# Optimization experiments

Measured on AMD Instinct MI355X. Metric: run time of the kernel, lower is better.

## Reference

```python
import jax, jax.numpy as jnp
import numpy as np

B, C, H, W = 16, 256, 64, 64
NH = 4                      # num_heads
HD = C // NH                # head_dim = 64
G = 32                      # GroupNorm groups
EPS = 1e-5


def setup_inputs() -> dict:
    key = jax.random.key(0)
    ks = jax.random.split(key, 7)
    x = jax.random.normal(ks[0], (B, C, H, W), dtype=jnp.float32)
    gn_w = jnp.ones((C,), dtype=jnp.float32)
    gn_b = jnp.zeros((C,), dtype=jnp.float32)
    qkv_w = jax.random.normal(ks[1], (3 * C, C), dtype=jnp.float32) * 0.02
    qkv_b = jnp.zeros((3 * C,), dtype=jnp.float32)
    out_w = jax.random.normal(ks[2], (C, C), dtype=jnp.float32) * 0.02
    out_b = jnp.zeros((C,), dtype=jnp.float32)
    return {"x": x, "gn_w": gn_w, "gn_b": gn_b, "qkv_w": qkv_w,
            "qkv_b": qkv_b, "out_w": out_w, "out_b": out_b}


def _group_norm(x, w, b):
    # x: (B, C, H, W); normalize over each of G groups of channels (+ spatial)
    Bx, Cx, Hx, Wx = x.shape
    xr = x.reshape(Bx, G, -1)
    mean = xr.mean(axis=-1, keepdims=True)
    var = xr.var(axis=-1, keepdims=True)
    h = ((xr - mean) * jax.lax.rsqrt(var + EPS)).reshape(Bx, Cx, Hx, Wx)
    return h * w[None, :, None, None] + b[None, :, None, None]


def reference(x, gn_w, gn_b, qkv_w, qkv_b, out_w, out_b):
    Bx, Cx, Hx, Wx = x.shape
    N = Hx * Wx
    h = _group_norm(x, gn_w, gn_b)
    # 1x1 conv == channel matmul
    qkv = jnp.einsum('oc,bchw->bohw', qkv_w, h) + qkv_b[None, :, None, None]
    q, k, v = jnp.split(qkv, 3, axis=1)
    # b (h d) y x -> b h d n
    q = q.reshape(Bx, NH, HD, N)
    k = k.reshape(Bx, NH, HD, N)
    v = v.reshape(Bx, NH, HD, N)
    q = jax.nn.softmax(q, axis=-1)   # over spatial positions n
    k = jax.nn.softmax(k, axis=-2)   # over head_dim d
    # context = k @ v^T : (b,h,d,d)
    context = jnp.einsum('bhdn,bhen->bhde', k, v)
    # out = context^T @ q : (b,h,d,n)
    out = jnp.einsum('bhde,bhdn->bhen', context, q)
    out = out.reshape(Bx, Cx, Hx, Wx)
    out = jnp.einsum('oc,bchw->bohw', out_w, out) + out_b[None, :, None, None]
    return x + out
```

## Files before the change

### kernel.cpp

```cpp
#include <hip/hip_runtime.h>


typedef __bf16 bf16x8 __attribute__((ext_vector_type(8)));
typedef __bf16 bf16x4 __attribute__((ext_vector_type(4)));
typedef __bf16 bf16x2 __attribute__((ext_vector_type(2)));
typedef float  f32x4  __attribute__((ext_vector_type(4)));

__device__ __forceinline__ float wave_red_sum(float v) {
#pragma unroll
    for (int off = 32; off > 0; off >>= 1) v += __shfl_xor(v, off, 64);
    return v;
}
__device__ __forceinline__ float wave_red_max(float v) {
#pragma unroll
    for (int off = 32; off > 0; off >>= 1) v = fmaxf(v, __shfl_xor(v, off, 64));
    return v;
}

__global__ __launch_bounds__(256)
void gn_stats_kernel(const float* __restrict__ x, const float* __restrict__ gw,
                     const float* __restrict__ gb, const float* __restrict__ qw,
                     float2* __restrict__ scsh, __bf16* __restrict__ wb)
{
    const int blk = blockIdx.x;
    const int b = blk >> 5, g = blk & 31;
    const int tid = threadIdx.x;
    const int lane = tid & 63, wid = tid >> 6;
    const size_t xbase = ((size_t)(b * 256 + g * 8)) * 4096;

    {
        const int ci = (blk * 256 + tid) * 2;
        if (ci < 196608) {
            const float2 f = *(const float2*)(qw + ci);
            bf16x2 t; t[0] = (__bf16)f.x; t[1] = (__bf16)f.y;
            *(bf16x2*)(wb + ci) = t;
        }
    }

    float s1 = 0.f, s2 = 0.f;
#pragma unroll
    for (int it = 0; it < 32; it++) {
        const int idx = (it * 256 + tid) * 4;
        const float4 v4 = *(const float4*)(x + xbase + idx);
        s1 += v4.x + v4.y + v4.z + v4.w;
        s2 += v4.x * v4.x + v4.y * v4.y + v4.z * v4.z + v4.w * v4.w;
    }
    __shared__ float red[8];
    float s1w = wave_red_sum(s1);
    float s2w = wave_red_sum(s2);
    if (lane == 0) { red[wid] = s1w; red[4 + wid] = s2w; }
    __syncthreads();
    const float mean = (red[0] + red[1] + red[2] + red[3]) * (1.0f / 32768.0f);
    const float ms   = (red[4] + red[5] + red[6] + red[7]) * (1.0f / 32768.0f);
    const float inv  = rsqrtf(fmaxf(ms - mean * mean, 0.f) + 1e-5f);

    if (tid < 8) {
        const int c = g * 8 + tid;
        const float sc = gw[c] * inv;
        const float sh = gb[c] - mean * sc;
        scsh[b * 256 + c] = make_float2(sc, sh);
    }
}

__global__ __launch_bounds__(256)
void gemm1_kernel(const __bf16* __restrict__ wbf,
                  const float* __restrict__ x,
                  const float* __restrict__ bias,
                  const float2* __restrict__ scsh,
                  __bf16* __restrict__ qkv)
{
    __shared__ __align__(16) __bf16 lds_bt[128 * 264];
    __shared__ __align__(16) __bf16 lds_a[128 * 40];
    __shared__ float2 lscsh[256];

    const int tid  = threadIdx.x;
    const int lane = tid & 63;
    const int wid  = tid >> 6;
    const int quad = lane >> 4;
    const int tcol = lane & 15;
    const int wm   = (wid & 1) * 64;
    const int wn   = (wid >> 1) * 64;
    const int n0   = blockIdx.x * 128;
    const int b    = n0 >> 12;
    const int nn   = n0 & 4095;

    lscsh[tid] = scsh[b * 256 + tid];
    __syncthreads();

    const int sn    = tid & 127;
    const int chalf = tid >> 7;
    const int swz   = (sn >> 3) & 3;
    const float* xs = x + (size_t)b * 1048576 + nn + sn;
#pragma unroll
    for (int iter = 0; iter < 8; iter++) {
        const int cbase = iter * 32 + chalf * 16;
        bf16x8 o0, o1;
#pragma unroll
        for (int j = 0; j < 16; j++) {
            const int c = cbase + j;
            const float2 ss = lscsh[c];
            const float f = xs[(size_t)c * 4096];
            const __bf16 v = (__bf16)(f * ss.x + ss.y);
            if (j < 8) o0[j] = v; else o1[j - 8] = v;
        }
        const int chunk = iter * 2 + chalf;
        const int chSw  = chunk ^ swz;
        __bf16* dst = &lds_bt[sn * 264 + chSw * 16];
        *(bf16x8*)dst       = o0;
        *(bf16x8*)(dst + 8) = o1;
    }

    const int arow = tid >> 1, k16 = (tid & 1) * 16;
    const __bf16* asrc0 = wbf + (size_t)arow * 256 + k16;

    for (int mt = 0; mt < 6; mt++) {
        const int m0 = mt * 128;
        f32x4 acc[4][4];
#pragma unroll
        for (int i = 0; i < 4; i++)
#pragma unroll
            for (int j = 0; j < 4; j++) acc[i][j] = {0.f, 0.f, 0.f, 0.f};

        const __bf16* asrc = asrc0 + (size_t)m0 * 256;
        bf16x8 a0 = *(const bf16x8*)(asrc);
        bf16x8 a1 = *(const bf16x8*)(asrc + 8);

        for (int kt = 0; kt < 256; kt += 32) {
            __syncthreads();
            *(bf16x8*)&lds_a[arow * 40 + k16]     = a0;
            *(bf16x8*)&lds_a[arow * 40 + k16 + 8] = a1;
            if (kt < 224) {
                const __bf16* an = asrc + kt + 32;
                a0 = *(const bf16x8*)(an);
                a1 = *(const bf16x8*)(an + 8);
            }
            __syncthreads();

            bf16x8 af[4];
#pragma unroll
            for (int mi = 0; mi < 4; mi++)
                af[mi] = *(const bf16x8*)&lds_a[(wm + mi * 16 + tcol) * 40 + quad * 8];
            bf16x8 bfr[4];
#pragma unroll
            for (int ni = 0; ni < 4; ni++) {
                const int n = wn + ni * 16 + tcol;
                const int k = kt + quad * 8;
                const int chSw2 = (k >> 4) ^ ((n >> 3) & 3);
                bfr[ni] = *(const bf16x8*)&lds_bt[n * 264 + chSw2 * 16 + (k & 15)];
            }
#pragma unroll
            for (int mi = 0; mi < 4; mi++)
#pragma unroll
                for (int ni = 0; ni < 4; ni++)
                    acc[mi][ni] = __builtin_amdgcn_mfma_f32_16x16x32_bf16(
                        af[mi], bfr[ni], acc[mi][ni], 0, 0, 0);
        }

#pragma unroll
        for (int mi = 0; mi < 4; mi++) {
#pragma unroll
            for (int r = 0; r < 4; r++) {
                const int grow = m0 + wm + mi * 16 + quad * 4 + r;
                const float bv = bias[grow];
#pragma unroll
                for (int ni = 0; ni < 4; ni++) {
                    const int gcol = n0 + wn + ni * 16 + tcol;
                    qkv[(size_t)grow * 65536 + gcol] = (__bf16)(acc[mi][ni][r] + bv);
                }
            }
        }
    }
}

__global__ __launch_bounds__(256)
void qstats_kernel(const __bf16* __restrict__ qkv, float2* __restrict__ qst)
{
    const int o = blockIdx.x >> 4;
    const int b = blockIdx.x & 15;
    const int tid = threadIdx.x;
    const int lane = tid & 63, wid = tid >> 6;
    const size_t base = (size_t)o * 65536 + (size_t)b * 4096;

    float v[16];
    float m = -INFINITY;
#pragma unroll
    for (int s = 0; s < 16; s++) {
        v[s] = (float)qkv[base + s * 256 + tid];
        m = fmaxf(m, v[s]);
    }
    __shared__ float red[4];
    float wmx = wave_red_max(m);
    if (lane == 0) red[wid] = wmx;
    __syncthreads();
    m = fmaxf(fmaxf(red[0], red[1]), fmaxf(red[2], red[3]));
    __syncthreads();
    float sum = 0.f;
#pragma unroll
    for (int s = 0; s < 16; s++) sum += __expf(v[s] - m);
    float wsm = wave_red_sum(sum);
    if (lane == 0) red[wid] = wsm;
    __syncthreads();
    if (tid == 0)
        qst[o * 16 + b] = make_float2(m, 1.0f / (red[0] + red[1] + red[2] + red[3]));
}

__global__ __launch_bounds__(256)
void ctx_mfma_kernel(const __bf16* __restrict__ qkv, float* __restrict__ ctx)
{
    const int bh = blockIdx.x >> 3, kc = blockIdx.x & 7;
    const int b = bh >> 2, hh = bh & 3;
    __shared__ __align__(16) __bf16 lk[64 * 72], lv[64 * 72];
    __shared__ float smax[4][64], ssum[4][64];
    const int tid = threadIdx.x;
    const int lane = tid & 63, wid = tid >> 6;
    const int quad = lane >> 4, tcol = lane & 15;
    const int eh = (wid & 1) * 32, dh = (wid >> 1) * 32;
    const int col = tid & 63, dq = tid >> 6;
    const int sd = tid >> 2, snn = (tid & 3) * 16;

    f32x4 acc[2][2];
#pragma unroll
    for (int i = 0; i < 2; i++)
#pragma unroll
        for (int j = 0; j < 2; j++) acc[i][j] = {0.f, 0.f, 0.f, 0.f};

    const size_t kbase = (size_t)(256 + hh * 64) * 65536 + (size_t)b * 4096 + kc * 512;
    const size_t vbase = (size_t)(512 + hh * 64) * 65536 + (size_t)b * 4096 + kc * 512;

    for (int nc = 0; nc < 512; nc += 64) {
        __syncthreads();
        {
            const __bf16* ks = qkv + kbase + (size_t)sd * 65536 + nc + snn;
            *(bf16x8*)&lk[sd * 72 + snn]     = *(const bf16x8*)ks;
            *(bf16x8*)&lk[sd * 72 + snn + 8] = *(const bf16x8*)(ks + 8);
            const __bf16* vs = qkv + vbase + (size_t)sd * 65536 + nc + snn;
            *(bf16x8*)&lv[sd * 72 + snn]     = *(const bf16x8*)vs;
            *(bf16x8*)&lv[sd * 72 + snn + 8] = *(const bf16x8*)(vs + 8);
        }
        __syncthreads();

        float kvv[16];
        float pm = -INFINITY;
#pragma unroll
        for (int i = 0; i < 16; i++) {
            kvv[i] = (float)lk[(dq * 16 + i) * 72 + col];
            pm = fmaxf(pm, kvv[i]);
        }
        smax[dq][col] = pm;
        __syncthreads();
        const float m = fmaxf(fmaxf(smax[0][col], smax[1][col]),
                              fmaxf(smax[2][col], smax[3][col]));
        float ps = 0.f;
#pragma unroll
        for (int i = 0; i < 16; i++) { kvv[i] = __expf(kvv[i] - m); ps += kvv[i]; }
        ssum[dq][col] = ps;
        __syncthreads();
        const float inv = 1.0f / (ssum[0][col] + ssum[1][col] + ssum[2][col] + ssum[3][col]);
#pragma unroll
        for (int i = 0; i < 16; i++)
            lk[(dq * 16 + i) * 72 + col] = (__bf16)(kvv[i] * inv);
        __syncthreads();

#pragma unroll
        for (int k2 = 0; k2 < 64; k2 += 32) {
            bf16x8 af[2], bfr[2];
#pragma unroll
            for (int mi = 0; mi < 2; mi++)
                af[mi] = *(const bf16x8*)&lv[(eh + mi * 16 + tcol) * 72 + k2 + quad * 8];
#pragma unroll
            for (int ni = 0; ni < 2; ni++)
                bfr[ni] = *(const bf16x8*)&lk[(dh + ni * 16 + tcol) * 72 + k2 + quad * 8];
#pragma unroll
            for (int mi = 0; mi < 2; mi++)
#pragma unroll
                for (int ni = 0; ni < 2; ni++)
                    acc[mi][ni] = __builtin_amdgcn_mfma_f32_16x16x32_bf16(
                        af[mi], bfr[ni], acc[mi][ni], 0, 0, 0);
        }
    }
    float* cb = ctx + (size_t)bh * 4096;
#pragma unroll
    for (int mi = 0; mi < 2; mi++)
#pragma unroll
        for (int ni = 0; ni < 2; ni++)
#pragma unroll
            for (int r = 0; r < 4; r++) {
                const int e = eh + mi * 16 + quad * 4 + r;
                const int d = dh + ni * 16 + tcol;
                atomicAdd(&cb[e * 64 + d], acc[mi][ni][r]);
            }
}

__global__ __launch_bounds__(256)
void w2_kernel(const float* __restrict__ ctx, const float* __restrict__ out_w,
               __bf16* __restrict__ w2)
{
    const int bh = blockIdx.x;
    const int b = bh >> 2, hh = bh & 3;
    const int tid = threadIdx.x;

    __shared__ __align__(16) float lctx[4096];
    const float* csrc = ctx + (size_t)bh * 4096;
#pragma unroll
    for (int i = 0; i < 4; i++)
        ((float4*)lctx)[tid + i * 256] = ((const float4*)csrc)[tid + i * 256];
    __syncthreads();

    float acc[64];
#pragma unroll
    for (int d = 0; d < 64; d++) acc[d] = 0.f;

    const float* wrow = out_w + (size_t)tid * 256 + hh * 64;
    for (int e = 0; e < 64; e++) {
        const float w = wrow[e];
#pragma unroll
        for (int d4 = 0; d4 < 64; d4 += 4) {
            const float4 c4 = *(const float4*)&lctx[e * 64 + d4];
            acc[d4 + 0] += w * c4.x;
            acc[d4 + 1] += w * c4.y;
            acc[d4 + 2] += w * c4.z;
            acc[d4 + 3] += w * c4.w;
        }
    }
    __bf16* dst = w2 + (size_t)b * 65536 + (size_t)tid * 256 + hh * 64;
#pragma unroll
    for (int d4 = 0; d4 < 64; d4 += 4) {
        bf16x4 t;
        t[0] = (__bf16)acc[d4 + 0]; t[1] = (__bf16)acc[d4 + 1];
        t[2] = (__bf16)acc[d4 + 2]; t[3] = (__bf16)acc[d4 + 3];
        *(bf16x4*)(dst + d4) = t;
    }
}

__global__ __launch_bounds__(256)
void gemm2_kernel(const __bf16* __restrict__ w2,
                  const __bf16* __restrict__ qkv,
                  const float2* __restrict__ qst,
                  const float* __restrict__ bias,
                  const float* __restrict__ xres,
                  float* __restrict__ out)
{
    __shared__ __align__(16) __bf16 lds_bt[128 * 264];
    __shared__ __align__(16) __bf16 lds_a[128 * 40];
    __shared__ float2 lqst[256];

    const int tid  = threadIdx.x;
    const int lane = tid & 63;
    const int wid  = tid >> 6;
    const int quad = lane >> 4;
    const int tcol = lane & 15;
    const int wm   = (wid & 1) * 64;
    const int wn   = (wid >> 1) * 64;
    const int n0   = blockIdx.x * 128;
    const int b    = n0 >> 12;

    lqst[tid] = qst[tid * 16 + b];
    __syncthreads();

    const int sn    = tid & 127;
    const int chalf = tid >> 7;
    const int swz   = (sn >> 3) & 3;
#pragma unroll
    for (int iter = 0; iter < 8; iter++) {
        const int cbase = iter * 32 + chalf * 16;
        bf16x8 o0, o1;
        const __bf16* qs = qkv + n0 + sn;
#pragma unroll
        for (int j = 0; j < 16; j++) {
            const int c = cbase + j;
            const float2 qq = lqst[c];
            const float f = (float)qs[(size_t)c * 65536];
            const __bf16 v = (__bf16)(__expf(f - qq.x) * qq.y);
            if (j < 8) o0[j] = v; else o1[j - 8] = v;
        }
        const int chunk = iter * 2 + chalf;
        const int chSw  = chunk ^ swz;
        __bf16* dst = &lds_bt[sn * 264 + chSw * 16];
        *(bf16x8*)dst       = o0;
        *(bf16x8*)(dst + 8) = o1;
    }

    const int arow = tid >> 1, k16 = (tid & 1) * 16;

    for (int mt = 0; mt < 2; mt++) {
        const int m0 = mt * 128;
        f32x4 acc[4][4];
#pragma unroll
        for (int i = 0; i < 4; i++)
#pragma unroll
            for (int j = 0; j < 4; j++) acc[i][j] = {0.f, 0.f, 0.f, 0.f};

        for (int kt = 0; kt < 256; kt += 32) {
            __syncthreads();
            {
                const __bf16* src = w2 + (size_t)b * 65536
                                  + (size_t)(m0 + arow) * 256 + kt + k16;
                const bf16x8 o0 = *(const bf16x8*)(src);
                const bf16x8 o1 = *(const bf16x8*)(src + 8);
                *(bf16x8*)&lds_a[arow * 40 + k16]     = o0;
                *(bf16x8*)&lds_a[arow * 40 + k16 + 8] = o1;
            }
            __syncthreads();

            bf16x8 af[4];
#pragma unroll
            for (int mi = 0; mi < 4; mi++)
                af[mi] = *(const bf16x8*)&lds_a[(wm + mi * 16 + tcol) * 40 + quad * 8];
            bf16x8 bfr[4];
#pragma unroll
            for (int ni = 0; ni < 4; ni++) {
                const int n = wn + ni * 16 + tcol;
                const int k = kt + quad * 8;
                const int chSw = (k >> 4) ^ ((n >> 3) & 3);
                bfr[ni] = *(const bf16x8*)&lds_bt[n * 264 + chSw * 16 + (k & 15)];
            }
#pragma unroll
            for (int mi = 0; mi < 4; mi++)
#pragma unroll
                for (int ni = 0; ni < 4; ni++)
                    acc[mi][ni] = __builtin_amdgcn_mfma_f32_16x16x32_bf16(
                        af[mi], bfr[ni], acc[mi][ni], 0, 0, 0);
        }

#pragma unroll
        for (int mi = 0; mi < 4; mi++) {
#pragma unroll
            for (int r = 0; r < 4; r++) {
                const int grow = m0 + wm + mi * 16 + quad * 4 + r;
                const float bv = bias[grow];
#pragma unroll
                for (int ni = 0; ni < 4; ni++) {
                    const int gcol = n0 + wn + ni * 16 + tcol;
                    const int n = gcol & 4095;
                    const size_t oidx = ((size_t)(b * 256 + grow)) * 4096 + n;
                    out[oidx] = acc[mi][ni][r] + bv + xres[oidx];
                }
            }
        }
    }
}

extern "C" void kernel_launch(void* const* d_in, const int* in_sizes, int n_in,
                              void* d_out, int out_size, void* d_ws, size_t ws_size,
                              hipStream_t stream)
{
    const float* x     = (const float*)d_in[0];
    const float* gn_w  = (const float*)d_in[1];
    const float* gn_b  = (const float*)d_in[2];
    const float* qkv_w = (const float*)d_in[3];
    const float* qkv_b = (const float*)d_in[4];
    const float* out_w = (const float*)d_in[5];
    const float* out_b = (const float*)d_in[6];
    float* out = (float*)d_out;

    char* ws = (char*)d_ws;
    __bf16* qkv  = (__bf16*)ws;
    float*  ctx  = (float*)(ws + (size_t)100663296);
    float2* scsh = (float2*)(ws + (size_t)101711872);
    float2* qst  = (float2*)(ws + (size_t)101744640);
    __bf16* wbf  = (__bf16*)(ws + (size_t)101777408);
    __bf16* w2   = qkv + (size_t)256 * 65536;

    hipMemsetAsync(ctx, 0, 262144 * sizeof(float), stream);
    gn_stats_kernel<<<512, 256, 0, stream>>>(x, gn_w, gn_b, qkv_w, scsh, wbf);
    gemm1_kernel<<<512, 256, 0, stream>>>(wbf, x, qkv_b, scsh, qkv);
    qstats_kernel<<<4096, 256, 0, stream>>>(qkv, qst);
    ctx_mfma_kernel<<<512, 256, 0, stream>>>(qkv, ctx);
    w2_kernel<<<64, 256, 0, stream>>>(ctx, out_w, w2);
    gemm2_kernel<<<512, 256, 0, stream>>>(w2, qkv, qst, out_b, x, out);
}
```

Baseline: 255.1 us.

## Load GEMM A fragments directly from global into registers, drop LDS staging

In both GEMM kernels the weight (A) tiles are no longer staged through LDS. Each wave now loads its MFMA A fragments straight from global memory into registers, prefetching one k-step ahead, which removes the two __syncthreads per k-iteration and the LDS write/read traffic. The XOR swizzle on the B tile in LDS is also dropped in favour of a plain padded row layout (stride 264). The cost is redundant global/L2 reads of weight rows across the waves sharing them, uncoalesced 16-byte per-lane loads, and possible LDS bank conflicts without the swizzle.

```diff
diff --git a/kernel.cpp b/kernel.cpp
--- a/kernel.cpp
+++ b/kernel.cpp
@@ -70,7 +70,6 @@
                   __bf16* __restrict__ qkv)
 {
     __shared__ __align__(16) __bf16 lds_bt[128 * 264];
-    __shared__ __align__(16) __bf16 lds_a[128 * 40];
     __shared__ float2 lscsh[256];
 
     const int tid  = threadIdx.x;
@@ -89,7 +88,6 @@
 
     const int sn    = tid & 127;
     const int chalf = tid >> 7;
-    const int swz   = (sn >> 3) & 3;
     const float* xs = x + (size_t)b * 1048576 + nn + sn;
 #pragma unroll
     for (int iter = 0; iter < 8; iter++) {
@@ -103,15 +101,13 @@
             const __bf16 v = (__bf16)(f * ss.x + ss.y);
             if (j < 8) o0[j] = v; else o1[j - 8] = v;
         }
-        const int chunk = iter * 2 + chalf;
-        const int chSw  = chunk ^ swz;
-        __bf16* dst = &lds_bt[sn * 264 + chSw * 16];
+        __bf16* dst = &lds_bt[sn * 264 + cbase];
         *(bf16x8*)dst       = o0;
         *(bf16x8*)(dst + 8) = o1;
     }
-
-    const int arow = tid >> 1, k16 = (tid & 1) * 16;
-    const __bf16* asrc0 = wbf + (size_t)arow * 256 + k16;
+    __syncthreads();
+
+    const __bf16* arow = wbf + (size_t)(wm + tcol) * 256 + quad * 8;
 
     for (int mt = 0; mt < 6; mt++) {
         const int m0 = mt * 128;
@@ -121,33 +117,26 @@
 #pragma unroll
             for (int j = 0; j < 4; j++) acc[i][j] = {0.f, 0.f, 0.f, 0.f};
 
-        const __bf16* asrc = asrc0 + (size_t)m0 * 256;
-        bf16x8 a0 = *(const bf16x8*)(asrc);
-        bf16x8 a1 = *(const bf16x8*)(asrc + 8);
+        const __bf16* ap = arow + (size_t)m0 * 256;
+        bf16x8 an[4];
+#pragma unroll
+        for (int mi = 0; mi < 4; mi++)
+            an[mi] = *(const bf16x8*)(ap + mi * 4096);
 
         for (int kt = 0; kt < 256; kt += 32) {
-            __syncthreads();
-            *(bf16x8*)&lds_a[arow * 40 + k16]     = a0;
-            *(bf16x8*)&lds_a[arow * 40 + k16 + 8] = a1;
+            bf16x8 af[4];
+#pragma unroll
+            for (int mi = 0; mi < 4; mi++) af[mi] = an[mi];
             if (kt < 224) {
-                const __bf16* an = asrc + kt + 32;
-                a0 = *(const bf16x8*)(an);
-                a1 = *(const bf16x8*)(an + 8);
+#pragma unroll
+                for (int mi = 0; mi < 4; mi++)
+                    an[mi] = *(const bf16x8*)(ap + mi * 4096 + kt + 32);
             }
-            __syncthreads();
-
-            bf16x8 af[4];
-#pragma unroll
-            for (int mi = 0; mi < 4; mi++)
-                af[mi] = *(const bf16x8*)&lds_a[(wm + mi * 16 + tcol) * 40 + quad * 8];
             bf16x8 bfr[4];
 #pragma unroll
-            for (int ni = 0; ni < 4; ni++) {
-                const int n = wn + ni * 16 + tcol;
-                const int k = kt + quad * 8;
-                const int chSw2 = (k >> 4) ^ ((n >> 3) & 3);
-                bfr[ni] = *(const bf16x8*)&lds_bt[n * 264 + chSw2 * 16 + (k & 15)];
-            }
+            for (int ni = 0; ni < 4; ni++)
+                bfr[ni] = *(const bf16x8*)&lds_bt[(wn + ni * 16 + tcol) * 264
+                                                 + kt + quad * 8];
 #pragma unroll
             for (int mi = 0; mi < 4; mi++)
 #pragma unroll
@@ -341,7 +330,6 @@
                   float* __restrict__ out)
 {
     __shared__ __align__(16) __bf16 lds_bt[128 * 264];
-    __shared__ __align__(16) __bf16 lds_a[128 * 40];
     __shared__ float2 lqst[256];
 
     const int tid  = threadIdx.x;
@@ -359,7 +347,6 @@
 
     const int sn    = tid & 127;
     const int chalf = tid >> 7;
-    const int swz   = (sn >> 3) & 3;
 #pragma unroll
     for (int iter = 0; iter < 8; iter++) {
         const int cbase = iter * 32 + chalf * 16;
@@ -373,14 +360,13 @@
             const __bf16 v = (__bf16)(__expf(f - qq.x) * qq.y);
             if (j < 8) o0[j] = v; else o1[j - 8] = v;
         }
-        const int chunk = iter * 2 + chalf;
-        const int chSw  = chunk ^ swz;
-        __bf16* dst = &lds_bt[sn * 264 + chSw * 16];
+        __bf16* dst = &lds_bt[sn * 264 + cbase];
         *(bf16x8*)dst       = o0;
         *(bf16x8*)(dst + 8) = o1;
     }
-
-    const int arow = tid >> 1, k16 = (tid & 1) * 16;
+    __syncthreads();
+
+    const __bf16* arow = w2 + (size_t)b * 65536 + (size_t)(wm + tcol) * 256 + quad * 8;
 
     for (int mt = 0; mt < 2; mt++) {
         const int m0 = mt * 128;
@@ -390,30 +376,26 @@
 #pragma unroll
             for (int j = 0; j < 4; j++) acc[i][j] = {0.f, 0.f, 0.f, 0.f};
 
+        const __bf16* ap = arow + (size_t)m0 * 256;
+        bf16x8 an[4];
+#pragma unroll
+        for (int mi = 0; mi < 4; mi++)
+            an[mi] = *(const bf16x8*)(ap + mi * 4096);
+
         for (int kt = 0; kt < 256; kt += 32) {
-            __syncthreads();
-            {
-                const __bf16* src = w2 + (size_t)b * 65536
-                                  + (size_t)(m0 + arow) * 256 + kt + k16;
-                const bf16x8 o0 = *(const bf16x8*)(src);
-                const bf16x8 o1 = *(const bf16x8*)(src + 8);
-                *(bf16x8*)&lds_a[arow * 40 + k16]     = o0;
-                *(bf16x8*)&lds_a[arow * 40 + k16 + 8] = o1;
+            bf16x8 af[4];
+#pragma unroll
+            for (int mi = 0; mi < 4; mi++) af[mi] = an[mi];
+            if (kt < 224) {
+#pragma unroll
+                for (int mi = 0; mi < 4; mi++)
+                    an[mi] = *(const bf16x8*)(ap + mi * 4096 + kt + 32);
             }
-            __syncthreads();
-
-            bf16x8 af[4];
-#pragma unroll
-            for (int mi = 0; mi < 4; mi++)
-                af[mi] = *(const bf16x8*)&lds_a[(wm + mi * 16 + tcol) * 40 + quad * 8];
             bf16x8 bfr[4];
 #pragma unroll
-            for (int ni = 0; ni < 4; ni++) {
-                const int n = wn + ni * 16 + tcol;
-                const int k = kt + quad * 8;
-                const int chSw = (k >> 4) ^ ((n >> 3) & 3);
-                bfr[ni] = *(const bf16x8*)&lds_bt[n * 264 + chSw * 16 + (k & 15)];
-            }
+            for (int ni = 0; ni < 4; ni++)
+                bfr[ni] = *(const bf16x8*)&lds_bt[(wn + ni * 16 + tcol) * 264
+                                                 + kt + quad * 8];
 #pragma unroll
             for (int mi = 0; mi < 4; mi++)
 #pragma unroll
```

Measured after the change: 320.4 us. 1.26x slower.

## Retile QKV GEMM to 256x64 blocks with swizzled A tile and cross-tile prefetch

Applied to the files above, without the earlier changes.

The QKV projection GEMM moves from 128x128 output tiles (2x2 wave grid, 6 M-tiles) to 256x64 tiles, with each wave owning 64 rows across all 64 columns, over 3 M-tiles. Grid size doubles to 1024 blocks. The weight tile is now stored in LDS as an unpadded 64-byte row with a rotate swizzle, and the next weight chunk is prefetched across M-tile boundaries. The intent is more blocks for occupancy, smaller LDS use and continuous prefetch. The cost is that each block re-reads the full weight matrix for only 64 columns, and the B-tile swizzle is removed, so LDS bank conflicts may appear on the 264-stride rows.

```diff
diff --git a/kernel.cpp b/kernel.cpp
--- a/kernel.cpp
+++ b/kernel.cpp
@@ -69,8 +69,8 @@
                   const float2* __restrict__ scsh,
                   __bf16* __restrict__ qkv)
 {
-    __shared__ __align__(16) __bf16 lds_bt[128 * 264];
-    __shared__ __align__(16) __bf16 lds_a[128 * 40];
+    __shared__ __align__(16) __bf16 lds_bt[64 * 264];
+    __shared__ __align__(16) char  lds_a[256 * 64];
     __shared__ float2 lscsh[256];
 
     const int tid  = threadIdx.x;
@@ -78,22 +78,20 @@
     const int wid  = tid >> 6;
     const int quad = lane >> 4;
     const int tcol = lane & 15;
-    const int wm   = (wid & 1) * 64;
-    const int wn   = (wid >> 1) * 64;
-    const int n0   = blockIdx.x * 128;
+    const int wm   = wid * 64;
+    const int n0   = blockIdx.x * 64;
     const int b    = n0 >> 12;
     const int nn   = n0 & 4095;
 
     lscsh[tid] = scsh[b * 256 + tid];
     __syncthreads();
 
-    const int sn    = tid & 127;
-    const int chalf = tid >> 7;
-    const int swz   = (sn >> 3) & 3;
+    const int sn = tid & 63;
+    const int cq = tid >> 6;
     const float* xs = x + (size_t)b * 1048576 + nn + sn;
 #pragma unroll
-    for (int iter = 0; iter < 8; iter++) {
-        const int cbase = iter * 32 + chalf * 16;
+    for (int iter = 0; iter < 4; iter++) {
+        const int cbase = cq * 64 + iter * 16;
         bf16x8 o0, o1;
 #pragma unroll
         for (int j = 0; j < 16; j++) {
@@ -103,51 +101,62 @@
             const __bf16 v = (__bf16)(f * ss.x + ss.y);
             if (j < 8) o0[j] = v; else o1[j - 8] = v;
         }
-        const int chunk = iter * 2 + chalf;
-        const int chSw  = chunk ^ swz;
-        __bf16* dst = &lds_bt[sn * 264 + chSw * 16];
+        __bf16* dst = &lds_bt[sn * 264 + cbase];
         *(bf16x8*)dst       = o0;
         *(bf16x8*)(dst + 8) = o1;
     }
 
-    const int arow = tid >> 1, k16 = (tid & 1) * 16;
-    const __bf16* asrc0 = wbf + (size_t)arow * 256 + k16;
-
-    for (int mt = 0; mt < 6; mt++) {
-        const int m0 = mt * 128;
+    const int r_   = tid >> 1;
+    const int ah   = tid & 1;
+    const int h16  = ah * 16;
+    const int aswz = (r_ >> 1) & 3;
+    const int ch0  = (((ah * 2)     + aswz) & 3) * 16;
+    const int ch1  = (((ah * 2 + 1) + aswz) & 3) * 16;
+    const __bf16* abase = wbf + (size_t)r_ * 256 + h16;
+
+    bf16x8 a0 = *(const bf16x8*)(abase);
+    bf16x8 a1 = *(const bf16x8*)(abase + 8);
+    bf16x8 a2 = *(const bf16x8*)(abase + 32768);
+    bf16x8 a3 = *(const bf16x8*)(abase + 32768 + 8);
+
+    for (int mt = 0; mt < 3; mt++) {
         f32x4 acc[4][4];
 #pragma unroll
         for (int i = 0; i < 4; i++)
 #pragma unroll
             for (int j = 0; j < 4; j++) acc[i][j] = {0.f, 0.f, 0.f, 0.f};
-
-        const __bf16* asrc = asrc0 + (size_t)m0 * 256;
-        bf16x8 a0 = *(const bf16x8*)(asrc);
-        bf16x8 a1 = *(const bf16x8*)(asrc + 8);
 
         for (int kt = 0; kt < 256; kt += 32) {
             __syncthreads();
-            *(bf16x8*)&lds_a[arow * 40 + k16]     = a0;
-            *(bf16x8*)&lds_a[arow * 40 + k16 + 8] = a1;
-            if (kt < 224) {
-                const __bf16* an = asrc + kt + 32;
-                a0 = *(const bf16x8*)(an);
-                a1 = *(const bf16x8*)(an + 8);
-            }
+            *(bf16x8*)&lds_a[r_ * 64         + ch0] = a0;
+            *(bf16x8*)&lds_a[r_ * 64         + ch1] = a1;
+            *(bf16x8*)&lds_a[(r_ + 128) * 64 + ch0] = a2;
+            *(bf16x8*)&lds_a[(r_ + 128) * 64 + ch1] = a3;
             __syncthreads();
 
+            const int last = (kt == 224);
+            const int nkt  = last ? 0 : kt + 32;
+            const int nmt  = last ? mt + 1 : mt;
+            if (nmt < 3) {
+                const __bf16* ap = abase + (size_t)nmt * 65536 + nkt;
+                a0 = *(const bf16x8*)(ap);
+                a1 = *(const bf16x8*)(ap + 8);
+                a2 = *(const bf16x8*)(ap + 32768);
+                a3 = *(const bf16x8*)(ap + 32768 + 8);
+            }
+
             bf16x8 af[4];
 #pragma unroll
-            for (int mi = 0; mi < 4; mi++)
-                af[mi] = *(const bf16x8*)&lds_a[(wm + mi * 16 + tcol) * 40 + quad * 8];
+            for (int mi = 0; mi < 4; mi++) {
+                const int m = wm + mi * 16 + tcol;
+                af[mi] = *(const bf16x8*)&lds_a[m * 64
+                         + ((quad + ((m >> 1) & 3)) & 3) * 16];
+            }
             bf16x8 bfr[4];
 #pragma unroll
-            for (int ni = 0; ni < 4; ni++) {
-                const int n = wn + ni * 16 + tcol;
-                const int k = kt + quad * 8;
-                const int chSw2 = (k >> 4) ^ ((n >> 3) & 3);
-                bfr[ni] = *(const bf16x8*)&lds_bt[n * 264 + chSw2 * 16 + (k & 15)];
-            }
+            for (int ni = 0; ni < 4; ni++)
+                bfr[ni] = *(const bf16x8*)&lds_bt[(ni * 16 + tcol) * 264
+                                                 + kt + quad * 8];
 #pragma unroll
             for (int mi = 0; mi < 4; mi++)
 #pragma unroll
@@ -160,11 +169,11 @@
         for (int mi = 0; mi < 4; mi++) {
 #pragma unroll
             for (int r = 0; r < 4; r++) {
-                const int grow = m0 + wm + mi * 16 + quad * 4 + r;
+                const int grow = mt * 256 + wm + mi * 16 + quad * 4 + r;
                 const float bv = bias[grow];
 #pragma unroll
                 for (int ni = 0; ni < 4; ni++) {
-                    const int gcol = n0 + wn + ni * 16 + tcol;
+                    const int gcol = n0 + ni * 16 + tcol;
                     qkv[(size_t)grow * 65536 + gcol] = (__bf16)(acc[mi][ni][r] + bv);
                 }
             }
@@ -463,7 +472,7 @@
 
     hipMemsetAsync(ctx, 0, 262144 * sizeof(float), stream);
     gn_stats_kernel<<<512, 256, 0, stream>>>(x, gn_w, gn_b, qkv_w, scsh, wbf);
-    gemm1_kernel<<<512, 256, 0, stream>>>(wbf, x, qkv_b, scsh, qkv);
+    gemm1_kernel<<<1024, 256, 0, stream>>>(wbf, x, qkv_b, scsh, qkv);
     qstats_kernel<<<4096, 256, 0, stream>>>(qkv, qst);
     ctx_mfma_kernel<<<512, 256, 0, stream>>>(qkv, ctx);
     w2_kernel<<<64, 256, 0, stream>>>(ctx, out_w, w2);
```

New measurement: 265.5 us. +4.1%, slower.
